# Kernel tuning notes

Hardware: AMD Instinct MI355X
Metric: run time of the kernel (lower is better)

The kernel has to match this reference:

```python
import jax, jax.numpy as jnp
import numpy as np

N_NODES = 50000
N_EDGES = 800000
D_IN, D_HID, D_OUT = 128, 256, 128


def setup_inputs() -> dict:
    key = jax.random.key(0)
    ks = jax.random.split(key, 8)
    x = jax.random.normal(ks[0], (N_NODES, D_IN), dtype=jnp.float32)
    edge_index = jax.random.randint(ks[1], (2, N_EDGES), 0, N_NODES, dtype=jnp.int64)
    # Xavier-ish scale for stability
    W_l1 = jax.random.normal(ks[2], (D_HID, D_IN), dtype=jnp.float32) * (1.0 / np.sqrt(D_IN))
    b_l1 = jnp.zeros((D_HID,), dtype=jnp.float32)
    W_r1 = jax.random.normal(ks[3], (D_HID, D_IN), dtype=jnp.float32) * (1.0 / np.sqrt(D_IN))
    W_l2 = jax.random.normal(ks[4], (D_OUT, D_HID), dtype=jnp.float32) * (1.0 / np.sqrt(D_HID))
    b_l2 = jnp.zeros((D_OUT,), dtype=jnp.float32)
    W_r2 = jax.random.normal(ks[5], (D_OUT, D_HID), dtype=jnp.float32) * (1.0 / np.sqrt(D_HID))
    return {"x": x, "edge_index": edge_index, "W_l1": W_l1, "b_l1": b_l1,
            "W_r1": W_r1, "W_l2": W_l2, "b_l2": b_l2, "W_r2": W_r2}


def _sage_conv(x, src, dst, W_l, b_l, W_r):
    # SAGEConv (aggr='mean', root_weight=True, normalize=False):
    #   out_i = W_l @ mean_{j in N(i)} x_j + b_l + W_r @ x_i
    n = x.shape[0]
    msgs = x[src]                                             # [E, d] gather
    agg = jax.ops.segment_sum(msgs, dst, num_segments=n)      # [N, d] scatter-add
    deg = jax.ops.segment_sum(jnp.ones((src.shape[0],), x.dtype), dst,
                              num_segments=n)
    agg = agg / jnp.maximum(deg, 1.0)[:, None]                # mean (0 for isolated)
    return agg @ W_l.T + b_l + x @ W_r.T


def reference(x, edge_index, W_l1, b_l1, W_r1, W_l2, b_l2, W_r2):
    # Note: PyG BasicGNN with num_layers=1 and jk=None applies NO activation
    # after its single conv, so the stack is two bare SAGEConv layers.
    src, dst = edge_index[0], edge_index[1]
    h = _sage_conv(x, src, dst, W_l1, b_l1, W_r1)
    out = _sage_conv(h, src, dst, W_l2, b_l2, W_r2)
    return out
```

## Files before the change

### kernel.cpp

```cpp
#include <hip/hip_runtime.h>

typedef __attribute__((ext_vector_type(4))) float f32x4;
typedef __attribute__((ext_vector_type(8))) short bf16x8;

__device__ inline ushort f2bf(float f) {
    uint u = __builtin_bit_cast(uint, f);
    u += 0x7fff + ((u >> 16) & 1);
    return (ushort)(u >> 16);
}
__device__ inline float bf2f(ushort h) {
    uint u = ((uint)h) << 16;
    return __builtin_bit_cast(float, u);
}

__global__ __launch_bounds__(256) void k_hist(const int* __restrict__ ei,
                                              int* __restrict__ cnt, int nE) {
    int e = blockIdx.x * 256 + threadIdx.x;
    if (e < nE) atomicAdd(&cnt[ei[nE + e]], 1);
}

__global__ __launch_bounds__(1024) void k_scan1(const int* __restrict__ cnt,
                                                int* __restrict__ rp,
                                                int* __restrict__ bsum, int n) {
    __shared__ int buf[1024];
    const int tid = threadIdx.x;
    const int i = blockIdx.x * 1024 + tid;
    int v = (i < n) ? cnt[i] : 0;
    buf[tid] = v;
    __syncthreads();
    #pragma unroll
    for (int off = 1; off < 1024; off <<= 1) {
        int t = 0;
        if (tid >= off) t = buf[tid - off];
        __syncthreads();
        if (tid >= off) buf[tid] += t;
        __syncthreads();
    }
    if (i < n) rp[i] = buf[tid] - v;
    if (tid == 1023) bsum[blockIdx.x] = buf[1023];
}

__global__ void k_scan2(const int* __restrict__ bsum, int* __restrict__ bofs,
                        int* __restrict__ rp, int nb, int n) {
    if (threadIdx.x == 0 && blockIdx.x == 0) {
        int run = 0;
        for (int b = 0; b < nb; ++b) { bofs[b] = run; run += bsum[b]; }
        rp[n] = run;
    }
}

__global__ __launch_bounds__(1024) void k_scan3(int* __restrict__ rp,
                                                const int* __restrict__ bofs, int n) {
    int i = blockIdx.x * 1024 + threadIdx.x;
    if (i < n) rp[i] += bofs[blockIdx.x];
}

__global__ __launch_bounds__(256) void k_fill(const int* __restrict__ ei,
                                              const int* __restrict__ rp,
                                              int* __restrict__ cur,
                                              int* __restrict__ srt, int nE) {
    int e = blockIdx.x * 256 + threadIdx.x;
    if (e >= nE) return;
    int d = ei[nE + e];
    int pos = rp[d] + atomicAdd(&cur[d], 1);
    srt[pos] = ei[e];
}

__global__ __launch_bounds__(256) void k_cvt_x(const float* __restrict__ x,
                                               ushort* __restrict__ A1, int n) {
    int e4 = blockIdx.x * 256 + threadIdx.x;
    if (e4 >= n * 32) return;
    int i = e4 >> 5, c4 = e4 & 31;
    float4 v = *(const float4*)(x + (size_t)i * 128 + c4 * 4);
    ushort4 o;
    o.x = f2bf(v.x); o.y = f2bf(v.y); o.z = f2bf(v.z); o.w = f2bf(v.w);
    *(ushort4*)(A1 + (size_t)i * 256 + 128 + c4 * 4) = o;
}

__global__ __launch_bounds__(256) void k_cvt_w(
    const float* __restrict__ Wl1, const float* __restrict__ Wr1,
    const float* __restrict__ Wl2, const float* __restrict__ Wr2,
    ushort* __restrict__ W1cat, ushort* __restrict__ W2cat) {
    int t = blockIdx.x * 256 + threadIdx.x;
    int which = t >> 14;
    int r = (t >> 6) & 255;
    int kq = t & 63;
    const float* src;
    ushort* dst;
    if (which == 0) {
        src = (kq < 32) ? (Wl1 + (size_t)r * 128 + kq * 4)
                        : (Wr1 + (size_t)r * 128 + (kq - 32) * 4);
        dst = W1cat + (size_t)r * 256 + kq * 4;
    } else {
        src = (r < 128) ? (Wl2 + (size_t)r * 256 + kq * 4)
                        : (Wr2 + (size_t)(r - 128) * 256 + kq * 4);
        dst = W2cat + (size_t)r * 256 + kq * 4;
    }
    float4 v = *(const float4*)src;
    ushort4 o;
    o.x = f2bf(v.x); o.y = f2bf(v.y); o.z = f2bf(v.z); o.w = f2bf(v.w);
    *(ushort4*)dst = o;
}

__global__ __launch_bounds__(256) void k_gather1(ushort* A1,
                                                 const int* __restrict__ srt,
                                                 const int* __restrict__ rp, int n) {
    const int node = blockIdx.x * 4 + (threadIdx.x >> 6);
    if (node >= n) return;
    const int lane = threadIdx.x & 63;
    const int beg = rp[node], end = rp[node + 1];
    float ax = 0.f, ay = 0.f;
    int e = beg;
    for (; e + 3 < end; e += 4) {
        int s0 = srt[e], s1 = srt[e + 1], s2 = srt[e + 2], s3 = srt[e + 3];
        uint v0 = *(const uint*)(A1 + (size_t)s0 * 256 + 128 + lane * 2);
        uint v1 = *(const uint*)(A1 + (size_t)s1 * 256 + 128 + lane * 2);
        uint v2 = *(const uint*)(A1 + (size_t)s2 * 256 + 128 + lane * 2);
        uint v3 = *(const uint*)(A1 + (size_t)s3 * 256 + 128 + lane * 2);
        ax += (bf2f((ushort)v0) + bf2f((ushort)v1)) + (bf2f((ushort)v2) + bf2f((ushort)v3));
        ay += (bf2f((ushort)(v0 >> 16)) + bf2f((ushort)(v1 >> 16)))
            + (bf2f((ushort)(v2 >> 16)) + bf2f((ushort)(v3 >> 16)));
    }
    for (; e < end; ++e) {
        uint v0 = *(const uint*)(A1 + (size_t)srt[e] * 256 + 128 + lane * 2);
        ax += bf2f((ushort)v0);
        ay += bf2f((ushort)(v0 >> 16));
    }
    const float invd = 1.0f / fmaxf((float)(end - beg), 1.0f);
    uint o = ((uint)f2bf(ay * invd) << 16) | (uint)f2bf(ax * invd);
    *(uint*)(A1 + (size_t)node * 256 + lane * 2) = o;
}

__global__ __launch_bounds__(256) void k_gather2(const ushort* __restrict__ H2,
                                                 const int* __restrict__ srt,
                                                 const int* __restrict__ rp,
                                                 const float* __restrict__ b2,
                                                 float* __restrict__ out, int n) {
    const int node = blockIdx.x * 4 + (threadIdx.x >> 6);
    if (node >= n) return;
    const int lane = threadIdx.x & 63;
    const int beg = rp[node], end = rp[node + 1];
    float ax = 0.f, ay = 0.f;
    int e = beg;
    for (; e + 3 < end; e += 4) {
        int s0 = srt[e], s1 = srt[e + 1], s2 = srt[e + 2], s3 = srt[e + 3];
        uint v0 = *(const uint*)(H2 + (size_t)s0 * 256 + lane * 2);
        uint v1 = *(const uint*)(H2 + (size_t)s1 * 256 + lane * 2);
        uint v2 = *(const uint*)(H2 + (size_t)s2 * 256 + lane * 2);
        uint v3 = *(const uint*)(H2 + (size_t)s3 * 256 + lane * 2);
        ax += (bf2f((ushort)v0) + bf2f((ushort)v1)) + (bf2f((ushort)v2) + bf2f((ushort)v3));
        ay += (bf2f((ushort)(v0 >> 16)) + bf2f((ushort)(v1 >> 16)))
            + (bf2f((ushort)(v2 >> 16)) + bf2f((ushort)(v3 >> 16)));
    }
    for (; e < end; ++e) {
        uint v0 = *(const uint*)(H2 + (size_t)srt[e] * 256 + lane * 2);
        ax += bf2f((ushort)v0);
        ay += bf2f((ushort)(v0 >> 16));
    }
    const float invd = 1.0f / fmaxf((float)(end - beg), 1.0f);
    uint rv = *(const uint*)(H2 + (size_t)node * 256 + 128 + lane * 2);
    float2 bb = *(const float2*)(b2 + lane * 2);
    float2 res;
    res.x = ax * invd + bf2f((ushort)rv) + bb.x;
    res.y = ay * invd + bf2f((ushort)(rv >> 16)) + bb.y;
    *(float2*)(out + (size_t)node * 128 + lane * 2) = res;
}

__global__ __launch_bounds__(512) void k_gemm_mfma(
    const ushort* __restrict__ A, const ushort* __restrict__ W,
    const float* __restrict__ bias, ushort* __restrict__ O, int n)
{
    __shared__ __align__(16) char sA[32768];
    const int bi = blockIdx.x * 64;
    const int tid = threadIdx.x;

    #pragma unroll
    for (int p = 0; p < 4; ++p) {
        const int o = p * 8192 + tid * 16;
        const int row = o >> 9;
        const int cb = o & 511;
        uint4 v = *(const uint4*)((const char*)A + (size_t)(bi + row) * 512 + cb);
        *(uint4*)(sA + row * 512 + (cb ^ ((row & 7) << 4))) = v;
    }
    __syncthreads();

    const int wid = tid >> 6;
    const int lane = tid & 63;
    const int wn = wid * 32;
    const int lr = lane & 15;
    const int lkb = (lane >> 4) * 16;

    f32x4 acc[4][2] = {};
    #pragma unroll
    for (int kk = 0; kk < 8; ++kk) {
        bf16x8 wf[2], af[4];
        #pragma unroll
        for (int ni = 0; ni < 2; ++ni)
            wf[ni] = *(const bf16x8*)((const char*)W + (size_t)(wn + ni * 16 + lr) * 512 + kk * 64 + lkb);
        #pragma unroll
        for (int mi = 0; mi < 4; ++mi) {
            const int row = mi * 16 + lr;
            const int cb = (kk * 64 + lkb) ^ ((row & 7) << 4);
            af[mi] = *(const bf16x8*)(sA + row * 512 + cb);
        }
        #pragma unroll
        for (int mi = 0; mi < 4; ++mi)
            #pragma unroll
            for (int ni = 0; ni < 2; ++ni)
                acc[mi][ni] = __builtin_amdgcn_mfma_f32_16x16x32_bf16(
                    af[mi], wf[ni], acc[mi][ni], 0, 0, 0);
    }

    const int crow0 = (lane >> 4) * 4;
    const int ccol = lane & 15;
    #pragma unroll
    for (int mi = 0; mi < 4; ++mi) {
        #pragma unroll
        for (int ni = 0; ni < 2; ++ni) {
            const int ocol = wn + ni * 16 + ccol;
            const float badd = bias ? bias[ocol] : 0.0f;
            #pragma unroll
            for (int j = 0; j < 4; ++j) {
                const int grow = bi + mi * 16 + crow0 + j;
                if (grow < n)
                    O[(size_t)grow * 256 + ocol] = f2bf(acc[mi][ni][j] + badd);
            }
        }
    }
}

extern "C" void kernel_launch(void* const* d_in, const int* in_sizes, int n_in,
                              void* d_out, int out_size, void* d_ws, size_t ws_size,
                              hipStream_t stream) {
    const float* x   = (const float*)d_in[0];
    const int*   ei  = (const int*)  d_in[1];
    const float* Wl1 = (const float*)d_in[2];
    const float* bl1 = (const float*)d_in[3];
    const float* Wr1 = (const float*)d_in[4];
    const float* Wl2 = (const float*)d_in[5];
    const float* bl2 = (const float*)d_in[6];
    const float* Wr2 = (const float*)d_in[7];
    float* out = (float*)d_out;

    const int nN = 50000;
    const int nE = in_sizes[1] / 2;

    char* ws = (char*)d_ws;
    int*    rp    = (int*)   (ws);
    int*    cnt   = (int*)   (ws + (size_t)256 * 1024);
    int*    cur   = (int*)   (ws + (size_t)456 * 1024);
    int*    bsum  = (int*)   (ws + (size_t)700 * 1024);
    int*    bofs  = (int*)   (ws + (size_t)700 * 1024 + 4096);
    int*    srt   = (int*)   (ws + (size_t)1 * (1 << 20));
    ushort* W1cat = (ushort*)(ws + (size_t)5 * (1 << 20));
    ushort* W2cat = (ushort*)(ws + (size_t)5 * (1 << 20) + 256 * 1024);
    ushort* A1    = (ushort*)(ws + (size_t)6 * (1 << 20));
    ushort* H     = (ushort*)(ws + (size_t)32 * (1 << 20));
    ushort* H2    = (ushort*)(ws + (size_t)58 * (1 << 20));

    const int nb = (nN + 1023) / 1024;

    hipMemsetAsync(cnt, 0, (size_t)(456 - 256 + 200) * 1024 - (456 - 256) * 1024 + (size_t)nN * 4, stream);
    hipMemsetAsync(cur, 0, (size_t)nN * 4, stream);
    k_hist<<<(nE + 255) / 256, 256, 0, stream>>>(ei, cnt, nE);
    k_scan1<<<nb, 1024, 0, stream>>>(cnt, rp, bsum, nN);
    k_scan2<<<1, 64, 0, stream>>>(bsum, bofs, rp, nb, nN);
    k_scan3<<<nb, 1024, 0, stream>>>(rp, bofs, nN);
    k_fill<<<(nE + 255) / 256, 256, 0, stream>>>(ei, rp, cur, srt, nE);

    k_cvt_x<<<(nN * 32 + 255) / 256, 256, 0, stream>>>(x, A1, nN);
    k_cvt_w<<<128, 256, 0, stream>>>(Wl1, Wr1, Wl2, Wr2, W1cat, W2cat);

    k_gather1<<<(nN + 3) / 4, 256, 0, stream>>>(A1, srt, rp, nN);
    k_gemm_mfma<<<(nN + 63) / 64, 512, 0, stream>>>(A1, W1cat, bl1, H, nN);

    k_gemm_mfma<<<(nN + 63) / 64, 512, 0, stream>>>(H, W2cat, nullptr, H2, nN);
    k_gather2<<<(nN + 3) / 4, 256, 0, stream>>>(H2, srt, rp, bl2, out, nN);
}
```

Before: 308.8 us.

## Fuse both GEMM layers, partition hist/fill atomics by node range, unroll gathers

```diff
diff --git a/kernel.cpp b/kernel.cpp
--- a/kernel.cpp
+++ b/kernel.cpp
@@ -13,10 +13,23 @@
     return __builtin_bit_cast(float, u);
 }
 
-__global__ __launch_bounds__(256) void k_hist(const int* __restrict__ ei,
-                                              int* __restrict__ cnt, int nE) {
-    int e = blockIdx.x * 256 + threadIdx.x;
-    if (e < nE) atomicAdd(&cnt[ei[nE + e]], 1);
+#define GRP 8
+#define NSLICE 6250
+#define CHUNK 2048
+
+__global__ __launch_bounds__(256) void k_hist_p(const int* __restrict__ ei,
+                                                int* __restrict__ cnt, int nE) {
+    const int g = blockIdx.x & 7;
+    const int c = blockIdx.x >> 3;
+    const int lo = g * NSLICE, hi = lo + NSLICE;
+    #pragma unroll
+    for (int p = 0; p < CHUNK / 256; ++p) {
+        int e = c * CHUNK + p * 256 + threadIdx.x;
+        if (e < nE) {
+            int d = ei[nE + e];
+            if (d >= lo && d < hi) atomicAdd(&cnt[d], 1);
+        }
+    }
 }
 
 __global__ __launch_bounds__(1024) void k_scan1(const int* __restrict__ cnt,
@@ -55,15 +68,25 @@
     if (i < n) rp[i] += bofs[blockIdx.x];
 }
 
-__global__ __launch_bounds__(256) void k_fill(const int* __restrict__ ei,
-                                              const int* __restrict__ rp,
-                                              int* __restrict__ cur,
-                                              int* __restrict__ srt, int nE) {
-    int e = blockIdx.x * 256 + threadIdx.x;
-    if (e >= nE) return;
-    int d = ei[nE + e];
-    int pos = rp[d] + atomicAdd(&cur[d], 1);
-    srt[pos] = ei[e];
+__global__ __launch_bounds__(256) void k_fill_p(const int* __restrict__ ei,
+                                                const int* __restrict__ rp,
+                                                int* __restrict__ cur,
+                                                int* __restrict__ srt, int nE) {
+    const int g = blockIdx.x & 7;
+    const int c = blockIdx.x >> 3;
+    const int lo = g * NSLICE, hi = lo + NSLICE;
+    #pragma unroll
+    for (int p = 0; p < CHUNK / 256; ++p) {
+        int e = c * CHUNK + p * 256 + threadIdx.x;
+        if (e < nE) {
+            int d = ei[nE + e];
+            int s = ei[e];
+            if (d >= lo && d < hi) {
+                int pos = rp[d] + atomicAdd(&cur[d], 1);
+                srt[pos] = s;
+            }
+        }
+    }
 }
 
 __global__ __launch_bounds__(256) void k_cvt_x(const float* __restrict__ x,
@@ -111,15 +134,16 @@
     const int beg = rp[node], end = rp[node + 1];
     float ax = 0.f, ay = 0.f;
     int e = beg;
-    for (; e + 3 < end; e += 4) {
-        int s0 = srt[e], s1 = srt[e + 1], s2 = srt[e + 2], s3 = srt[e + 3];
-        uint v0 = *(const uint*)(A1 + (size_t)s0 * 256 + 128 + lane * 2);
-        uint v1 = *(const uint*)(A1 + (size_t)s1 * 256 + 128 + lane * 2);
-        uint v2 = *(const uint*)(A1 + (size_t)s2 * 256 + 128 + lane * 2);
-        uint v3 = *(const uint*)(A1 + (size_t)s3 * 256 + 128 + lane * 2);
-        ax += (bf2f((ushort)v0) + bf2f((ushort)v1)) + (bf2f((ushort)v2) + bf2f((ushort)v3));
-        ay += (bf2f((ushort)(v0 >> 16)) + bf2f((ushort)(v1 >> 16)))
-            + (bf2f((ushort)(v2 >> 16)) + bf2f((ushort)(v3 >> 16)));
+    for (; e + 7 < end; e += 8) {
+        uint v[8];
+        #pragma unroll
+        for (int q = 0; q < 8; ++q)
+            v[q] = *(const uint*)(A1 + (size_t)srt[e + q] * 256 + 128 + lane * 2);
+        #pragma unroll
+        for (int q = 0; q < 8; ++q) {
+            ax += bf2f((ushort)v[q]);
+            ay += bf2f((ushort)(v[q] >> 16));
+        }
     }
     for (; e < end; ++e) {
         uint v0 = *(const uint*)(A1 + (size_t)srt[e] * 256 + 128 + lane * 2);
@@ -142,15 +166,16 @@
     const int beg = rp[node], end = rp[node + 1];
     float ax = 0.f, ay = 0.f;
     int e = beg;
-    for (; e + 3 < end; e += 4) {
-        int s0 = srt[e], s1 = srt[e + 1], s2 = srt[e + 2], s3 = srt[e + 3];
-        uint v0 = *(const uint*)(H2 + (size_t)s0 * 256 + lane * 2);
-        uint v1 = *(const uint*)(H2 + (size_t)s1 * 256 + lane * 2);
-        uint v2 = *(const uint*)(H2 + (size_t)s2 * 256 + lane * 2);
-        uint v3 = *(const uint*)(H2 + (size_t)s3 * 256 + lane * 2);
-        ax += (bf2f((ushort)v0) + bf2f((ushort)v1)) + (bf2f((ushort)v2) + bf2f((ushort)v3));
-        ay += (bf2f((ushort)(v0 >> 16)) + bf2f((ushort)(v1 >> 16)))
-            + (bf2f((ushort)(v2 >> 16)) + bf2f((ushort)(v3 >> 16)));
+    for (; e + 7 < end; e += 8) {
+        uint v[8];
+        #pragma unroll
+        for (int q = 0; q < 8; ++q)
+            v[q] = *(const uint*)(H2 + (size_t)srt[e + q] * 256 + lane * 2);
+        #pragma unroll
+        for (int q = 0; q < 8; ++q) {
+            ax += bf2f((ushort)v[q]);
+            ay += bf2f((ushort)(v[q] >> 16));
+        }
     }
     for (; e < end; ++e) {
         uint v0 = *(const uint*)(H2 + (size_t)srt[e] * 256 + lane * 2);
@@ -166,11 +191,13 @@
     *(float2*)(out + (size_t)node * 128 + lane * 2) = res;
 }
 
-__global__ __launch_bounds__(512) void k_gemm_mfma(
-    const ushort* __restrict__ A, const ushort* __restrict__ W,
-    const float* __restrict__ bias, ushort* __restrict__ O, int n)
+__global__ __launch_bounds__(512, 4) void k_gemm_fused(
+    const ushort* __restrict__ A, const ushort* __restrict__ W1,
+    const ushort* __restrict__ W2, const float* __restrict__ b1,
+    ushort* __restrict__ O, int n)
 {
     __shared__ __align__(16) char sA[32768];
+    __shared__ __align__(16) char sH[32768];
     const int bi = blockIdx.x * 64;
     const int tid = threadIdx.x;
 
@@ -189,43 +216,79 @@
     const int wn = wid * 32;
     const int lr = lane & 15;
     const int lkb = (lane >> 4) * 16;
-
-    f32x4 acc[4][2] = {};
-    #pragma unroll
-    for (int kk = 0; kk < 8; ++kk) {
-        bf16x8 wf[2], af[4];
-        #pragma unroll
-        for (int ni = 0; ni < 2; ++ni)
-            wf[ni] = *(const bf16x8*)((const char*)W + (size_t)(wn + ni * 16 + lr) * 512 + kk * 64 + lkb);
-        #pragma unroll
-        for (int mi = 0; mi < 4; ++mi) {
-            const int row = mi * 16 + lr;
-            const int cb = (kk * 64 + lkb) ^ ((row & 7) << 4);
-            af[mi] = *(const bf16x8*)(sA + row * 512 + cb);
-        }
-        #pragma unroll
-        for (int mi = 0; mi < 4; ++mi)
-            #pragma unroll
-            for (int ni = 0; ni < 2; ++ni)
-                acc[mi][ni] = __builtin_amdgcn_mfma_f32_16x16x32_bf16(
-                    af[mi], wf[ni], acc[mi][ni], 0, 0, 0);
-    }
-
     const int crow0 = (lane >> 4) * 4;
     const int ccol = lane & 15;
-    #pragma unroll
-    for (int mi = 0; mi < 4; ++mi) {
-        #pragma unroll
-        for (int ni = 0; ni < 2; ++ni) {
-            const int ocol = wn + ni * 16 + ccol;
-            const float badd = bias ? bias[ocol] : 0.0f;
-            #pragma unroll
-            for (int j = 0; j < 4; ++j) {
-                const int grow = bi + mi * 16 + crow0 + j;
-                if (grow < n)
-                    O[(size_t)grow * 256 + ocol] = f2bf(acc[mi][ni][j] + badd);
-            }
-        }
+
+    {
+        f32x4 acc[4][2] = {};
+        #pragma unroll
+        for (int kk = 0; kk < 8; ++kk) {
+            bf16x8 wf[2], af[4];
+            #pragma unroll
+            for (int ni = 0; ni < 2; ++ni)
+                wf[ni] = *(const bf16x8*)((const char*)W1 + (size_t)(wn + ni * 16 + lr) * 512 + kk * 64 + lkb);
+            #pragma unroll
+            for (int mi = 0; mi < 4; ++mi) {
+                const int row = mi * 16 + lr;
+                af[mi] = *(const bf16x8*)(sA + row * 512 + ((kk * 64 + lkb) ^ ((row & 7) << 4)));
+            }
+            #pragma unroll
+            for (int mi = 0; mi < 4; ++mi)
+                #pragma unroll
+                for (int ni = 0; ni < 2; ++ni)
+                    acc[mi][ni] = __builtin_amdgcn_mfma_f32_16x16x32_bf16(
+                        af[mi], wf[ni], acc[mi][ni], 0, 0, 0);
+        }
+        const float badd0 = b1[wn + ccol];
+        const float badd1 = b1[wn + 16 + ccol];
+        #pragma unroll
+        for (int mi = 0; mi < 4; ++mi)
+            #pragma unroll
+            for (int ni = 0; ni < 2; ++ni) {
+                const int col = wn + ni * 16 + ccol;
+                const float badd = ni ? badd1 : badd0;
+                #pragma unroll
+                for (int j = 0; j < 4; ++j) {
+                    const int row = mi * 16 + crow0 + j;
+                    *(ushort*)(sH + row * 512 + ((col * 2) ^ ((row & 7) << 4))) =
+                        f2bf(acc[mi][ni][j] + badd);
+                }
+            }
+    }
+    __syncthreads();
+
+    {
+        f32x4 acc[4][2] = {};
+        #pragma unroll
+        for (int kk = 0; kk < 8; ++kk) {
+            bf16x8 wf[2], af[4];
+            #pragma unroll
+            for (int ni = 0; ni < 2; ++ni)
+                wf[ni] = *(const bf16x8*)((const char*)W2 + (size_t)(wn + ni * 16 + lr) * 512 + kk * 64 + lkb);
+            #pragma unroll
+            for (int mi = 0; mi < 4; ++mi) {
+                const int row = mi * 16 + lr;
+                af[mi] = *(const bf16x8*)(sH + row * 512 + ((kk * 64 + lkb) ^ ((row & 7) << 4)));
+            }
+            #pragma unroll
+            for (int mi = 0; mi < 4; ++mi)
+                #pragma unroll
+                for (int ni = 0; ni < 2; ++ni)
+                    acc[mi][ni] = __builtin_amdgcn_mfma_f32_16x16x32_bf16(
+                        af[mi], wf[ni], acc[mi][ni], 0, 0, 0);
+        }
+        #pragma unroll
+        for (int mi = 0; mi < 4; ++mi)
+            #pragma unroll
+            for (int ni = 0; ni < 2; ++ni) {
+                const int ocol = wn + ni * 16 + ccol;
+                #pragma unroll
+                for (int j = 0; j < 4; ++j) {
+                    const int grow = bi + mi * 16 + crow0 + j;
+                    if (grow < n)
+                        O[(size_t)grow * 256 + ocol] = f2bf(acc[mi][ni][j]);
+                }
+            }
     }
 }
 
@@ -247,33 +310,31 @@
 
     char* ws = (char*)d_ws;
     int*    rp    = (int*)   (ws);
-    int*    cnt   = (int*)   (ws + (size_t)256 * 1024);
-    int*    cur   = (int*)   (ws + (size_t)456 * 1024);
-    int*    bsum  = (int*)   (ws + (size_t)700 * 1024);
-    int*    bofs  = (int*)   (ws + (size_t)700 * 1024 + 4096);
+    int*    cnt   = (int*)   (ws + 262144);
+    int*    cur   = (int*)   (ws + 524288);
+    int*    bsum  = (int*)   (ws + 786432);
+    int*    bofs  = (int*)   (ws + 790528);
     int*    srt   = (int*)   (ws + (size_t)1 * (1 << 20));
     ushort* W1cat = (ushort*)(ws + (size_t)5 * (1 << 20));
     ushort* W2cat = (ushort*)(ws + (size_t)5 * (1 << 20) + 256 * 1024);
     ushort* A1    = (ushort*)(ws + (size_t)6 * (1 << 20));
-    ushort* H     = (ushort*)(ws + (size_t)32 * (1 << 20));
-    ushort* H2    = (ushort*)(ws + (size_t)58 * (1 << 20));
+    ushort* H2    = (ushort*)(ws + (size_t)32 * (1 << 20));
 
     const int nb = (nN + 1023) / 1024;
-
-    hipMemsetAsync(cnt, 0, (size_t)(456 - 256 + 200) * 1024 - (456 - 256) * 1024 + (size_t)nN * 4, stream);
-    hipMemsetAsync(cur, 0, (size_t)nN * 4, stream);
-    k_hist<<<(nE + 255) / 256, 256, 0, stream>>>(ei, cnt, nE);
+    const int nChunks = (nE + CHUNK - 1) / CHUNK;
+
+    hipMemsetAsync(ws + 262144, 0, 462144, stream);
+    k_hist_p<<<nChunks * GRP, 256, 0, stream>>>(ei, cnt, nE);
     k_scan1<<<nb, 1024, 0, stream>>>(cnt, rp, bsum, nN);
     k_scan2<<<1, 64, 0, stream>>>(bsum, bofs, rp, nb, nN);
     k_scan3<<<nb, 1024, 0, stream>>>(rp, bofs, nN);
-    k_fill<<<(nE + 255) / 256, 256, 0, stream>>>(ei, rp, cur, srt, nE);
+    k_fill_p<<<nChunks * GRP, 256, 0, stream>>>(ei, rp, cur, srt, nE);
 
     k_cvt_x<<<(nN * 32 + 255) / 256, 256, 0, stream>>>(x, A1, nN);
     k_cvt_w<<<128, 256, 0, stream>>>(Wl1, Wr1, Wl2, Wr2, W1cat, W2cat);
 
     k_gather1<<<(nN + 3) / 4, 256, 0, stream>>>(A1, srt, rp, nN);
-    k_gemm_mfma<<<(nN + 63) / 64, 512, 0, stream>>>(A1, W1cat, bl1, H, nN);
-
-    k_gemm_mfma<<<(nN + 63) / 64, 512, 0, stream>>>(H, W2cat, nullptr, H2, nN);
+    k_gemm_fused<<<(nN + 63) / 64, 512, 0, stream>>>(A1, W1cat, W2cat, bl1, H2, nN);
+
     k_gather2<<<(nN + 3) / 4, 256, 0, stream>>>(H2, srt, rp, bl2, out, nN);
 }
```

Result: faster. 294.5 us (-4.6%).
